# Kernel optimization log

Measured on AMD Instinct MI355X. Metric: run time of the kernel, lower is better.

Reference implementation:

```python
import jax, jax.numpy as jnp
import numpy as np

N_NODES = 50000
N_EDGES = 800000
N_GRAPHS = 50
IN_FEATS = 128
H1_FEATS = 64
OUT_FEATS = 32
GAT_SLOPE = 0.2   # DGL GATConv default negative_slope
LRELU_SLOPE = 0.01  # F.leaky_relu default


def setup_inputs() -> dict:
    key = jax.random.key(0)
    ks = jax.random.split(key, 12)
    x = jax.random.normal(ks[0], (N_NODES, IN_FEATS), jnp.float32)
    src = jax.random.randint(ks[1], (N_EDGES,), 0, N_NODES)
    dst = jax.random.randint(ks[2], (N_EDGES,), 0, N_NODES)
    graph_id = jnp.sort(jax.random.randint(ks[3], (N_NODES,), 0, N_GRAPHS))
    s1 = 1.0 / np.sqrt(IN_FEATS)
    s2 = 1.0 / np.sqrt(H1_FEATS)
    W1 = jax.random.normal(ks[4], (IN_FEATS, H1_FEATS), jnp.float32) * s1
    al1 = jax.random.normal(ks[5], (H1_FEATS,), jnp.float32) * s2
    ar1 = jax.random.normal(ks[6], (H1_FEATS,), jnp.float32) * s2
    b1 = jnp.zeros((H1_FEATS,), jnp.float32)
    W2 = jax.random.normal(ks[7], (H1_FEATS, OUT_FEATS), jnp.float32) * s2
    al2 = jax.random.normal(ks[8], (OUT_FEATS,), jnp.float32) * (1.0 / np.sqrt(OUT_FEATS))
    ar2 = jax.random.normal(ks[9], (OUT_FEATS,), jnp.float32) * (1.0 / np.sqrt(OUT_FEATS))
    b2 = jnp.zeros((OUT_FEATS,), jnp.float32)
    return {"x": x, "src": src, "dst": dst, "graph_id": graph_id,
            "W1": W1, "al1": al1, "ar1": ar1, "b1": b1,
            "W2": W2, "al2": al2, "ar2": ar2, "b2": b2}


def _gat_layer(h, src, dst, W, al, ar, b, n_nodes):
    # single-head DGL GATConv (feat_drop=attn_drop=0, bias added post-aggregation)
    z = h @ W                                   # (N, out)
    el = z @ al                                 # (N,) left attention logits
    er = z @ ar                                 # (N,) right attention logits
    e = jax.nn.leaky_relu(el[src] + er[dst], GAT_SLOPE)     # (E,)
    m = jax.ops.segment_max(e, dst, num_segments=n_nodes)  # per-dst max for stable softmax
    p = jnp.exp(e - m[dst])
    s = jax.ops.segment_sum(p, dst, num_segments=n_nodes)
    alpha = p / s[dst]                          # edge softmax over incoming edges
    out = jax.ops.segment_sum(alpha[:, None] * z[src], dst, num_segments=n_nodes)
    return out + b


def reference(x, src, dst, graph_id, W1, al1, ar1, b1, W2, al2, ar2, b2):
    n = x.shape[0]
    h = jax.nn.leaky_relu(_gat_layer(x, src, dst, W1, al1, ar1, b1, n), LRELU_SLOPE)
    h = jax.nn.leaky_relu(_gat_layer(h, src, dst, W2, al2, ar2, b2, n), LRELU_SLOPE)
    # dgl.mean_nodes: per-graph mean over nodes
    cnt = jax.ops.segment_sum(jnp.ones((n,), h.dtype), graph_id, num_segments=N_GRAPHS)
    pooled = jax.ops.segment_sum(h, graph_id, num_segments=N_GRAPHS) / jnp.maximum(cnt, 1.0)[:, None]
    return pooled
```

## Files before the change

kernel.cpp:

```cpp
#include <hip/hip_runtime.h>
#include <math.h>

#define NN 50000
#define NE 800000
#define NG 50
#define F0 128
#define F1 64
#define F2 32
#define NPB 256
#define NBK 196
#define CHUNK 4096
#define NC 196

__device__ __forceinline__ float lrelu(float v, float slope) {
    return v > 0.0f ? v : v * slope;
}

__global__ __launch_bounds__(256) void gemm1_kernel(
    const float* __restrict__ x, const float* __restrict__ W,
    const float* __restrict__ al, const float* __restrict__ ar,
    float* __restrict__ z, float* __restrict__ el, float* __restrict__ er)
{
    __shared__ float Ws[F0 * F1];
    __shared__ float xs[32][F0];
    int tid = threadIdx.x;
    int r0 = blockIdx.x * 32;

    {
        const float4* W4 = reinterpret_cast<const float4*>(W);
        float4* Ws4 = reinterpret_cast<float4*>(Ws);
        #pragma unroll
        for (int i = 0; i < 8; ++i) Ws4[tid + i * 256] = W4[tid + i * 256];
    }
    {
        float4 zero = {0.f, 0.f, 0.f, 0.f};
        #pragma unroll
        for (int i = 0; i < 4; ++i) {
            int s = tid + i * 256;
            int row = s >> 5, c4 = s & 31;
            int grow = r0 + row;
            float4 v = (grow < NN)
                ? reinterpret_cast<const float4*>(x)[(size_t)grow * 32 + c4] : zero;
            *reinterpret_cast<float4*>(&xs[row][c4 * 4]) = v;
        }
    }
    __syncthreads();

    int j = tid & 63, rg = tid >> 6;
    float acc[8] = {0.f, 0.f, 0.f, 0.f, 0.f, 0.f, 0.f, 0.f};
    for (int k4 = 0; k4 < F0 / 4; ++k4) {
        float w0 = Ws[(k4 * 4 + 0) * F1 + j];
        float w1 = Ws[(k4 * 4 + 1) * F1 + j];
        float w2 = Ws[(k4 * 4 + 2) * F1 + j];
        float w3 = Ws[(k4 * 4 + 3) * F1 + j];
        #pragma unroll
        for (int r = 0; r < 8; ++r) {
            float4 xv = *reinterpret_cast<const float4*>(&xs[rg * 8 + r][k4 * 4]);
            acc[r] = fmaf(xv.x, w0, fmaf(xv.y, w1, fmaf(xv.z, w2, fmaf(xv.w, w3, acc[r]))));
        }
    }

    float a_l = al[j], a_r = ar[j];
    #pragma unroll
    for (int r = 0; r < 8; ++r) {
        int row = r0 + rg * 8 + r;
        if (row < NN) z[(size_t)row * F1 + j] = acc[r];
        float pl = acc[r] * a_l, pr = acc[r] * a_r;
        #pragma unroll
        for (int mm = 1; mm < 64; mm <<= 1) {
            pl += __shfl_xor(pl, mm);
            pr += __shfl_xor(pr, mm);
        }
        if (j == 0 && row < NN) { el[row] = pl; er[row] = pr; }
    }
}

__global__ __launch_bounds__(256) void gemm2_kernel(
    const float* __restrict__ h, const float* __restrict__ W,
    const float* __restrict__ al, const float* __restrict__ ar,
    float* __restrict__ z, float* __restrict__ el, float* __restrict__ er)
{
    __shared__ float Ws[F1 * F2];
    __shared__ float xs[64][F1];
    int tid = threadIdx.x;
    int r0 = blockIdx.x * 64;

    {
        const float4* W4 = reinterpret_cast<const float4*>(W);
        float4* Ws4 = reinterpret_cast<float4*>(Ws);
        #pragma unroll
        for (int i = 0; i < 2; ++i) Ws4[tid + i * 256] = W4[tid + i * 256];
    }
    {
        float4 zero = {0.f, 0.f, 0.f, 0.f};
        #pragma unroll
        for (int i = 0; i < 4; ++i) {
            int s = tid + i * 256;
            int row = s >> 4, c4 = s & 15;
            int grow = r0 + row;
            float4 v = (grow < NN)
                ? reinterpret_cast<const float4*>(h)[(size_t)grow * 16 + c4] : zero;
            *reinterpret_cast<float4*>(&xs[row][c4 * 4]) = v;
        }
    }
    __syncthreads();

    int j = tid & 31, rg = tid >> 5;
    float acc[8] = {0.f, 0.f, 0.f, 0.f, 0.f, 0.f, 0.f, 0.f};
    for (int k4 = 0; k4 < F1 / 4; ++k4) {
        float w0 = Ws[(k4 * 4 + 0) * F2 + j];
        float w1 = Ws[(k4 * 4 + 1) * F2 + j];
        float w2 = Ws[(k4 * 4 + 2) * F2 + j];
        float w3 = Ws[(k4 * 4 + 3) * F2 + j];
        #pragma unroll
        for (int r = 0; r < 8; ++r) {
            float4 xv = *reinterpret_cast<const float4*>(&xs[rg * 8 + r][k4 * 4]);
            acc[r] = fmaf(xv.x, w0, fmaf(xv.y, w1, fmaf(xv.z, w2, fmaf(xv.w, w3, acc[r]))));
        }
    }

    float a_l = al[j], a_r = ar[j];
    #pragma unroll
    for (int r = 0; r < 8; ++r) {
        int row = r0 + rg * 8 + r;
        if (row < NN) z[(size_t)row * F2 + j] = acc[r];
        float pl = acc[r] * a_l, pr = acc[r] * a_r;
        #pragma unroll
        for (int mm = 1; mm < 32; mm <<= 1) {
            pl += __shfl_xor(pl, mm);
            pr += __shfl_xor(pr, mm);
        }
        if (j == 0 && row < NN) { el[row] = pl; er[row] = pr; }
    }
}


__global__ __launch_bounds__(256) void p1_hist_kernel(
    const int* __restrict__ dst, int* __restrict__ hist)
{
    __shared__ int h[NBK];
    int c = blockIdx.x;
    if (threadIdx.x < NBK) h[threadIdx.x] = 0;
    __syncthreads();
    int e0 = c * CHUNK;
    int e1 = (e0 + CHUNK < NE) ? e0 + CHUNK : NE;
    for (int e = e0 + threadIdx.x; e < e1; e += 256)
        atomicAdd(&h[dst[e] >> 8], 1);
    __syncthreads();
    if (threadIdx.x < NBK) hist[threadIdx.x * NC + c] = h[threadIdx.x];
}

__global__ __launch_bounds__(256) void p2a_scan_kernel(
    int* __restrict__ hist, int* __restrict__ btot)
{
    __shared__ int t[256];
    int b = blockIdx.x;
    int v = (threadIdx.x < NC) ? hist[b * NC + threadIdx.x] : 0;
    t[threadIdx.x] = v;
    __syncthreads();
    for (int off = 1; off < 256; off <<= 1) {
        int u = (threadIdx.x >= off) ? t[threadIdx.x - off] : 0;
        __syncthreads();
        t[threadIdx.x] += u;
        __syncthreads();
    }
    if (threadIdx.x < NC) hist[b * NC + threadIdx.x] = t[threadIdx.x] - v;
    if (threadIdx.x == 255) btot[b] = t[255];
}

__global__ __launch_bounds__(256) void p2b_scan_kernel(
    const int* __restrict__ btot, int* __restrict__ bstart, int* __restrict__ row_start)
{
    __shared__ int t[256];
    int v = (threadIdx.x < NBK) ? btot[threadIdx.x] : 0;
    t[threadIdx.x] = v;
    __syncthreads();
    for (int off = 1; off < 256; off <<= 1) {
        int u = (threadIdx.x >= off) ? t[threadIdx.x - off] : 0;
        __syncthreads();
        t[threadIdx.x] += u;
        __syncthreads();
    }
    if (threadIdx.x < NBK) bstart[threadIdx.x] = t[threadIdx.x] - v;
    if (threadIdx.x == NBK) bstart[NBK] = NE;
    if (threadIdx.x == 0) row_start[NN] = NE;
}

__global__ __launch_bounds__(256) void p3_part_kernel(
    const int* __restrict__ src, const int* __restrict__ dst,
    const int* __restrict__ hist, const int* __restrict__ bstart,
    int2* __restrict__ part)
{
    __shared__ int base[NBK];
    __shared__ int cnt[NBK];
    int c = blockIdx.x;
    if (threadIdx.x < NBK) {
        base[threadIdx.x] = hist[threadIdx.x * NC + c] + bstart[threadIdx.x];
        cnt[threadIdx.x] = 0;
    }
    __syncthreads();
    int e0 = c * CHUNK;
    int e1 = (e0 + CHUNK < NE) ? e0 + CHUNK : NE;
    for (int e = e0 + threadIdx.x; e < e1; e += 256) {
        int s = src[e], d = dst[e];
        int b = d >> 8;
        int r = atomicAdd(&cnt[b], 1);
        part[base[b] + r] = make_int2(s, d);
    }
}

__global__ __launch_bounds__(256) void p4_fill_kernel(
    const int2* __restrict__ part, const int* __restrict__ bstart,
    int* __restrict__ row_start, int* __restrict__ srcs)
{
    __shared__ int deg[NPB];
    __shared__ int off[NPB];
    __shared__ int cnt[NPB];
    int b = blockIdx.x;
    int lo = bstart[b], hi = bstart[b + 1];
    deg[threadIdx.x] = 0;
    cnt[threadIdx.x] = 0;
    __syncthreads();
    for (int i = lo + threadIdx.x; i < hi; i += 256)
        atomicAdd(&deg[part[i].y & (NPB - 1)], 1);
    __syncthreads();
    int v = deg[threadIdx.x];
    off[threadIdx.x] = v;
    __syncthreads();
    for (int o = 1; o < 256; o <<= 1) {
        int u = (threadIdx.x >= o) ? off[threadIdx.x - o] : 0;
        __syncthreads();
        off[threadIdx.x] += u;
        __syncthreads();
    }
    int ex = off[threadIdx.x] - v;
    __syncthreads();
    off[threadIdx.x] = ex;
    __syncthreads();
    int node = b * NPB + threadIdx.x;
    if (node < NN) row_start[node] = lo + ex;
    for (int i = lo + threadIdx.x; i < hi; i += 256) {
        int2 e = part[i];
        int n = e.y & (NPB - 1);
        int r = atomicAdd(&cnt[n], 1);
        srcs[lo + off[n] + r] = e.x;
    }
}

__global__ __launch_bounds__(256) void gat_agg64_kernel(
    const int* __restrict__ row_start, const int* __restrict__ srcs,
    const float* __restrict__ el, const float* __restrict__ er,
    const float* __restrict__ z, const float* __restrict__ b,
    float* __restrict__ out, float slope_out)
{
    int node = (blockIdx.x * 256 + threadIdx.x) >> 6;
    if (node >= NN) return;
    int lane = threadIdx.x & 63;
    int g = lane >> 4, c = lane & 15;
    int beg = row_start[node], end = row_start[node + 1];
    float erd = er[node];

    int i0 = beg + lane;
    float v0 = -INFINITY;
    if (i0 < end) v0 = lrelu(el[srcs[i0]] + erd, 0.2f);
    float lm = v0;
    for (int i = i0 + 64; i < end; i += 64)
        lm = fmaxf(lm, lrelu(el[srcs[i]] + erd, 0.2f));
    #pragma unroll
    for (int mm = 1; mm < 64; mm <<= 1) lm = fmaxf(lm, __shfl_xor(lm, mm));

    float preg = 0.f, ls = 0.f;
    if (i0 < end) { preg = __expf(v0 - lm); ls = preg; }
    for (int i = i0 + 64; i < end; i += 64)
        ls += __expf(lrelu(el[srcs[i]] + erd, 0.2f) - lm);
    #pragma unroll
    for (int mm = 1; mm < 64; mm <<= 1) ls += __shfl_xor(ls, mm);
    float inv_s = (ls > 0.f) ? 1.0f / ls : 0.f;

    const float4* z4 = reinterpret_cast<const float4*>(z);
    float4 acc = {0.f, 0.f, 0.f, 0.f};
    for (int ib = beg; ib < end; ib += 4) {
        int i = ib + g;
        int j = i - beg;
        float pv = __shfl(preg, j & 63);
        if (i < end) {
            int sn = srcs[i];
            if (j >= 64) pv = __expf(lrelu(el[sn] + erd, 0.2f) - lm);
            float alpha = pv * inv_s;
            float4 zv = z4[(size_t)sn * 16 + c];
            acc.x = fmaf(alpha, zv.x, acc.x);
            acc.y = fmaf(alpha, zv.y, acc.y);
            acc.z = fmaf(alpha, zv.z, acc.z);
            acc.w = fmaf(alpha, zv.w, acc.w);
        }
    }
    #pragma unroll
    for (int mm = 16; mm < 64; mm <<= 1) {
        acc.x += __shfl_xor(acc.x, mm);
        acc.y += __shfl_xor(acc.y, mm);
        acc.z += __shfl_xor(acc.z, mm);
        acc.w += __shfl_xor(acc.w, mm);
    }
    if (g == 0) {
        float4 bb = reinterpret_cast<const float4*>(b)[c];
        float4 o;
        o.x = lrelu(acc.x + bb.x, slope_out);
        o.y = lrelu(acc.y + bb.y, slope_out);
        o.z = lrelu(acc.z + bb.z, slope_out);
        o.w = lrelu(acc.w + bb.w, slope_out);
        reinterpret_cast<float4*>(out)[(size_t)node * 16 + c] = o;
    }
}

__global__ __launch_bounds__(256) void gat_agg32_kernel(
    const int* __restrict__ row_start, const int* __restrict__ srcs,
    const float* __restrict__ el, const float* __restrict__ er,
    const float* __restrict__ z, const float* __restrict__ b,
    float* __restrict__ out, float slope_out)
{
    int node = (blockIdx.x * 256 + threadIdx.x) >> 5;
    if (node >= NN) return;
    int sub = threadIdx.x & 31;
    int base = threadIdx.x & 32;
    int g = sub >> 3, c = sub & 7;
    int beg = row_start[node], end = row_start[node + 1];
    float erd = er[node];

    int i0 = beg + sub;
    float v0 = -INFINITY;
    if (i0 < end) v0 = lrelu(el[srcs[i0]] + erd, 0.2f);
    float lm = v0;
    for (int i = i0 + 32; i < end; i += 32)
        lm = fmaxf(lm, lrelu(el[srcs[i]] + erd, 0.2f));
    #pragma unroll
    for (int mm = 1; mm < 32; mm <<= 1) lm = fmaxf(lm, __shfl_xor(lm, mm));

    float preg = 0.f, ls = 0.f;
    if (i0 < end) { preg = __expf(v0 - lm); ls = preg; }
    for (int i = i0 + 32; i < end; i += 32)
        ls += __expf(lrelu(el[srcs[i]] + erd, 0.2f) - lm);
    #pragma unroll
    for (int mm = 1; mm < 32; mm <<= 1) ls += __shfl_xor(ls, mm);
    float inv_s = (ls > 0.f) ? 1.0f / ls : 0.f;

    const float4* z4 = reinterpret_cast<const float4*>(z);
    float4 acc = {0.f, 0.f, 0.f, 0.f};
    for (int ib = beg; ib < end; ib += 4) {
        int i = ib + g;
        int j = i - beg;
        float pv = __shfl(preg, base | (j & 31));
        if (i < end) {
            int sn = srcs[i];
            if (j >= 32) pv = __expf(lrelu(el[sn] + erd, 0.2f) - lm);
            float alpha = pv * inv_s;
            float4 zv = z4[(size_t)sn * 8 + c];
            acc.x = fmaf(alpha, zv.x, acc.x);
            acc.y = fmaf(alpha, zv.y, acc.y);
            acc.z = fmaf(alpha, zv.z, acc.z);
            acc.w = fmaf(alpha, zv.w, acc.w);
        }
    }
    #pragma unroll
    for (int mm = 8; mm < 32; mm <<= 1) {
        acc.x += __shfl_xor(acc.x, mm);
        acc.y += __shfl_xor(acc.y, mm);
        acc.z += __shfl_xor(acc.z, mm);
        acc.w += __shfl_xor(acc.w, mm);
    }
    if (g == 0) {
        float4 bb = reinterpret_cast<const float4*>(b)[c];
        float4 o;
        o.x = lrelu(acc.x + bb.x, slope_out);
        o.y = lrelu(acc.y + bb.y, slope_out);
        o.z = lrelu(acc.z + bb.z, slope_out);
        o.w = lrelu(acc.w + bb.w, slope_out);
        reinterpret_cast<float4*>(out)[(size_t)node * 8 + c] = o;
    }
}

__global__ __launch_bounds__(256) void pool_kernel(
    const float* __restrict__ h2, const int* __restrict__ gid, float* __restrict__ out)
{
    int g = blockIdx.x;
    int lo = 0, hi = NN;
    while (lo < hi) { int mid = (lo + hi) >> 1; if (gid[mid] < g) lo = mid + 1; else hi = mid; }
    int start = lo;
    hi = NN;
    while (lo < hi) { int mid = (lo + hi) >> 1; if (gid[mid] < g + 1) lo = mid + 1; else hi = mid; }
    int end = lo;

    int f = threadIdx.x & 31, r = threadIdx.x >> 5;
    float acc = 0.f;
    for (int n = start + r; n < end; n += 8) acc += h2[(size_t)n * F2 + f];
    __shared__ float red[256];
    red[threadIdx.x] = acc;
    __syncthreads();
    for (int st = 128; st >= 32; st >>= 1) {
        if (threadIdx.x < st) red[threadIdx.x] += red[threadIdx.x + st];
        __syncthreads();
    }
    if (threadIdx.x < 32) {
        float cnt = (float)(end - start);
        out[g * F2 + threadIdx.x] = red[threadIdx.x] / fmaxf(cnt, 1.0f);
    }
}

extern "C" void kernel_launch(void* const* d_in, const int* in_sizes, int n_in,
                              void* d_out, int out_size, void* d_ws, size_t ws_size,
                              hipStream_t stream)
{
    const float* x   = (const float*)d_in[0];
    const int*   src = (const int*)d_in[1];
    const int*   dst = (const int*)d_in[2];
    const int*   gid = (const int*)d_in[3];
    const float* W1  = (const float*)d_in[4];
    const float* al1 = (const float*)d_in[5];
    const float* ar1 = (const float*)d_in[6];
    const float* b1  = (const float*)d_in[7];
    const float* W2  = (const float*)d_in[8];
    const float* al2 = (const float*)d_in[9];
    const float* ar2 = (const float*)d_in[10];
    const float* b2  = (const float*)d_in[11];
    float* out = (float*)d_out;

    float* ws   = (float*)d_ws;
    float* z1   = ws;
    float* h1   = z1 + (size_t)NN * F1;
    float* z2   = h1 + (size_t)NN * F1;
    float* h2   = z2 + (size_t)NN * F2;
    float* el   = h2 + (size_t)NN * F2;
    float* er   = el + NN;
    int* row_start = (int*)(er + NN);
    int* srcs      = row_start + NN + 1;
    int* hist      = srcs + NE;
    int* btot      = hist + NBK * NC;
    int* bstart    = btot + NBK;
    int2* part = reinterpret_cast<int2*>(z1);

    p1_hist_kernel<<<NC, 256, 0, stream>>>(dst, hist);
    p2a_scan_kernel<<<NBK, 256, 0, stream>>>(hist, btot);
    p2b_scan_kernel<<<1, 256, 0, stream>>>(btot, bstart, row_start);
    p3_part_kernel<<<NC, 256, 0, stream>>>(src, dst, hist, bstart, part);
    p4_fill_kernel<<<NBK, 256, 0, stream>>>(part, bstart, row_start, srcs);

    gemm1_kernel<<<(NN + 31) / 32, 256, 0, stream>>>(x, W1, al1, ar1, z1, el, er);
    gat_agg64_kernel<<<(NN * 64 + 255) / 256, 256, 0, stream>>>(
        row_start, srcs, el, er, z1, b1, h1, 0.01f);

    gemm2_kernel<<<(NN + 63) / 64, 256, 0, stream>>>(h1, W2, al2, ar2, z2, el, er);
    gat_agg32_kernel<<<(NN * 32 + 255) / 256, 256, 0, stream>>>(
        row_start, srcs, el, er, z2, b2, h2, 0.01f);

    pool_kernel<<<NG, 256, 0, stream>>>(h2, gid, out);
}
```

Before: 286.8 us.

## Fuse histogram into gemm1, drop bucket-scan kernel, unroll aggregation loops

The edge-destination histogram is merged into the first GEMM launch as extra blocks, so both run in one grid. The single-block bucket scan kernel is removed, and each partition/fill block recomputes the 196-entry prefix sum itself. The partition buffer moves out of z1 so it no longer aliases the GEMM output, which is what allows the fusion. The aggregation kernels pre-scale the softmax weights by the inverse sum and process two edges per iteration to expose more memory-level parallelism, at the cost of redundant scan work per block and more register pressure.

```diff
diff --git a/kernel.cpp b/kernel.cpp
--- a/kernel.cpp
+++ b/kernel.cpp
@@ -11,12 +11,15 @@
 #define NBK 196
 #define CHUNK 4096
 #define NC 196
+#define NTILE1 1563
+#define NTILE2 782
 
 __device__ __forceinline__ float lrelu(float v, float slope) {
     return v > 0.0f ? v : v * slope;
 }
 
-__global__ __launch_bounds__(256) void gemm1_kernel(
+__global__ __launch_bounds__(256) void k1_hist_gemm1_kernel(
+    const int* __restrict__ dst, int* __restrict__ hist,
     const float* __restrict__ x, const float* __restrict__ W,
     const float* __restrict__ al, const float* __restrict__ ar,
     float* __restrict__ z, float* __restrict__ el, float* __restrict__ er)
@@ -24,8 +27,22 @@
     __shared__ float Ws[F0 * F1];
     __shared__ float xs[32][F0];
     int tid = threadIdx.x;
-    int r0 = blockIdx.x * 32;
-
+
+    if (blockIdx.x < NC) {
+        int* h = (int*)Ws;
+        int c = blockIdx.x;
+        if (tid < NBK) h[tid] = 0;
+        __syncthreads();
+        int e0 = c * CHUNK;
+        int e1 = (e0 + CHUNK < NE) ? e0 + CHUNK : NE;
+        for (int e = e0 + tid; e < e1; e += 256)
+            atomicAdd(&h[dst[e] >> 8], 1);
+        __syncthreads();
+        if (tid < NBK) hist[tid * NC + c] = h[tid];
+        return;
+    }
+
+    int r0 = (blockIdx.x - NC) * 32;
     {
         const float4* W4 = reinterpret_cast<const float4*>(W);
         float4* Ws4 = reinterpret_cast<float4*>(Ws);
@@ -45,7 +62,6 @@
         }
     }
     __syncthreads();
-
     int j = tid & 63, rg = tid >> 6;
     float acc[8] = {0.f, 0.f, 0.f, 0.f, 0.f, 0.f, 0.f, 0.f};
     for (int k4 = 0; k4 < F0 / 4; ++k4) {
@@ -59,7 +75,6 @@
             acc[r] = fmaf(xv.x, w0, fmaf(xv.y, w1, fmaf(xv.z, w2, fmaf(xv.w, w3, acc[r]))));
         }
     }
-
     float a_l = al[j], a_r = ar[j];
     #pragma unroll
     for (int r = 0; r < 8; ++r) {
@@ -75,81 +90,6 @@
     }
 }
 
-__global__ __launch_bounds__(256) void gemm2_kernel(
-    const float* __restrict__ h, const float* __restrict__ W,
-    const float* __restrict__ al, const float* __restrict__ ar,
-    float* __restrict__ z, float* __restrict__ el, float* __restrict__ er)
-{
-    __shared__ float Ws[F1 * F2];
-    __shared__ float xs[64][F1];
-    int tid = threadIdx.x;
-    int r0 = blockIdx.x * 64;
-
-    {
-        const float4* W4 = reinterpret_cast<const float4*>(W);
-        float4* Ws4 = reinterpret_cast<float4*>(Ws);
-        #pragma unroll
-        for (int i = 0; i < 2; ++i) Ws4[tid + i * 256] = W4[tid + i * 256];
-    }
-    {
-        float4 zero = {0.f, 0.f, 0.f, 0.f};
-        #pragma unroll
-        for (int i = 0; i < 4; ++i) {
-            int s = tid + i * 256;
-            int row = s >> 4, c4 = s & 15;
-            int grow = r0 + row;
-            float4 v = (grow < NN)
-                ? reinterpret_cast<const float4*>(h)[(size_t)grow * 16 + c4] : zero;
-            *reinterpret_cast<float4*>(&xs[row][c4 * 4]) = v;
-        }
-    }
-    __syncthreads();
-
-    int j = tid & 31, rg = tid >> 5;
-    float acc[8] = {0.f, 0.f, 0.f, 0.f, 0.f, 0.f, 0.f, 0.f};
-    for (int k4 = 0; k4 < F1 / 4; ++k4) {
-        float w0 = Ws[(k4 * 4 + 0) * F2 + j];
-        float w1 = Ws[(k4 * 4 + 1) * F2 + j];
-        float w2 = Ws[(k4 * 4 + 2) * F2 + j];
-        float w3 = Ws[(k4 * 4 + 3) * F2 + j];
-        #pragma unroll
-        for (int r = 0; r < 8; ++r) {
-            float4 xv = *reinterpret_cast<const float4*>(&xs[rg * 8 + r][k4 * 4]);
-            acc[r] = fmaf(xv.x, w0, fmaf(xv.y, w1, fmaf(xv.z, w2, fmaf(xv.w, w3, acc[r]))));
-        }
-    }
-
-    float a_l = al[j], a_r = ar[j];
-    #pragma unroll
-    for (int r = 0; r < 8; ++r) {
-        int row = r0 + rg * 8 + r;
-        if (row < NN) z[(size_t)row * F2 + j] = acc[r];
-        float pl = acc[r] * a_l, pr = acc[r] * a_r;
-        #pragma unroll
-        for (int mm = 1; mm < 32; mm <<= 1) {
-            pl += __shfl_xor(pl, mm);
-            pr += __shfl_xor(pr, mm);
-        }
-        if (j == 0 && row < NN) { el[row] = pl; er[row] = pr; }
-    }
-}
-
-
-__global__ __launch_bounds__(256) void p1_hist_kernel(
-    const int* __restrict__ dst, int* __restrict__ hist)
-{
-    __shared__ int h[NBK];
-    int c = blockIdx.x;
-    if (threadIdx.x < NBK) h[threadIdx.x] = 0;
-    __syncthreads();
-    int e0 = c * CHUNK;
-    int e1 = (e0 + CHUNK < NE) ? e0 + CHUNK : NE;
-    for (int e = e0 + threadIdx.x; e < e1; e += 256)
-        atomicAdd(&h[dst[e] >> 8], 1);
-    __syncthreads();
-    if (threadIdx.x < NBK) hist[threadIdx.x * NC + c] = h[threadIdx.x];
-}
-
 __global__ __launch_bounds__(256) void p2a_scan_kernel(
     int* __restrict__ hist, int* __restrict__ btot)
 {
@@ -168,40 +108,33 @@
     if (threadIdx.x == 255) btot[b] = t[255];
 }
 
-__global__ __launch_bounds__(256) void p2b_scan_kernel(
-    const int* __restrict__ btot, int* __restrict__ bstart, int* __restrict__ row_start)
-{
-    __shared__ int t[256];
-    int v = (threadIdx.x < NBK) ? btot[threadIdx.x] : 0;
-    t[threadIdx.x] = v;
-    __syncthreads();
-    for (int off = 1; off < 256; off <<= 1) {
-        int u = (threadIdx.x >= off) ? t[threadIdx.x - off] : 0;
-        __syncthreads();
-        t[threadIdx.x] += u;
-        __syncthreads();
-    }
-    if (threadIdx.x < NBK) bstart[threadIdx.x] = t[threadIdx.x] - v;
-    if (threadIdx.x == NBK) bstart[NBK] = NE;
-    if (threadIdx.x == 0) row_start[NN] = NE;
-}
-
 __global__ __launch_bounds__(256) void p3_part_kernel(
     const int* __restrict__ src, const int* __restrict__ dst,
-    const int* __restrict__ hist, const int* __restrict__ bstart,
+    const int* __restrict__ hist, const int* __restrict__ btot,
     int2* __restrict__ part)
 {
+    __shared__ int t[256];
     __shared__ int base[NBK];
     __shared__ int cnt[NBK];
+    int tid = threadIdx.x;
     int c = blockIdx.x;
-    if (threadIdx.x < NBK) {
-        base[threadIdx.x] = hist[threadIdx.x * NC + c] + bstart[threadIdx.x];
-        cnt[threadIdx.x] = 0;
+    int v = (tid < NBK) ? btot[tid] : 0;
+    t[tid] = v;
+    __syncthreads();
+    for (int off = 1; off < 256; off <<= 1) {
+        int u = (tid >= off) ? t[tid - off] : 0;
+        __syncthreads();
+        t[tid] += u;
+        __syncthreads();
+    }
+    if (tid < NBK) {
+        base[tid] = hist[tid * NC + c] + (t[tid] - v);
+        cnt[tid] = 0;
     }
     __syncthreads();
     int e0 = c * CHUNK;
     int e1 = (e0 + CHUNK < NE) ? e0 + CHUNK : NE;
-    for (int e = e0 + threadIdx.x; e < e1; e += 256) {
+    for (int e = e0 + tid; e < e1; e += 256) {
         int s = src[e], d = dst[e];
         int b = d >> 8;
         int r = atomicAdd(&cnt[b], 1);
@@ -210,36 +143,49 @@
 }
 
 __global__ __launch_bounds__(256) void p4_fill_kernel(
-    const int2* __restrict__ part, const int* __restrict__ bstart,
+    const int2* __restrict__ part, const int* __restrict__ btot,
     int* __restrict__ row_start, int* __restrict__ srcs)
 {
+    __shared__ int t[256];
     __shared__ int deg[NPB];
     __shared__ int off[NPB];
     __shared__ int cnt[NPB];
+    int tid = threadIdx.x;
     int b = blockIdx.x;
-    int lo = bstart[b], hi = bstart[b + 1];
-    deg[threadIdx.x] = 0;
-    cnt[threadIdx.x] = 0;
-    __syncthreads();
-    for (int i = lo + threadIdx.x; i < hi; i += 256)
+    int v = (tid < NBK) ? btot[tid] : 0;
+    t[tid] = v;
+    __syncthreads();
+    for (int o = 1; o < 256; o <<= 1) {
+        int u = (tid >= o) ? t[tid - o] : 0;
+        __syncthreads();
+        t[tid] += u;
+        __syncthreads();
+    }
+    int hi = t[b];
+    int lo = hi - btot[b];
+    if (b == 0 && tid == 0) row_start[NN] = NE;
+    deg[tid] = 0;
+    cnt[tid] = 0;
+    __syncthreads();
+    for (int i = lo + tid; i < hi; i += 256)
         atomicAdd(&deg[part[i].y & (NPB - 1)], 1);
     __syncthreads();
-    int v = deg[threadIdx.x];
-    off[threadIdx.x] = v;
+    int dv = deg[tid];
+    off[tid] = dv;
     __syncthreads();
     for (int o = 1; o < 256; o <<= 1) {
-        int u = (threadIdx.x >= o) ? off[threadIdx.x - o] : 0;
-        __syncthreads();
-        off[threadIdx.x] += u;
-        __syncthreads();
-    }
-    int ex = off[threadIdx.x] - v;
-    __syncthreads();
-    off[threadIdx.x] = ex;
-    __syncthreads();
-    int node = b * NPB + threadIdx.x;
+        int u = (tid >= o) ? off[tid - o] : 0;
+        __syncthreads();
+        off[tid] += u;
+        __syncthreads();
+    }
+    int ex = off[tid] - dv;
+    __syncthreads();
+    off[tid] = ex;
+    __syncthreads();
+    int node = b * NPB + tid;
     if (node < NN) row_start[node] = lo + ex;
-    for (int i = lo + threadIdx.x; i < hi; i += 256) {
+    for (int i = lo + tid; i < hi; i += 256) {
         int2 e = part[i];
         int n = e.y & (NPB - 1);
         int r = atomicAdd(&cnt[n], 1);
@@ -276,22 +222,37 @@
     #pragma unroll
     for (int mm = 1; mm < 64; mm <<= 1) ls += __shfl_xor(ls, mm);
     float inv_s = (ls > 0.f) ? 1.0f / ls : 0.f;
+    preg *= inv_s;
 
     const float4* z4 = reinterpret_cast<const float4*>(z);
     float4 acc = {0.f, 0.f, 0.f, 0.f};
-    for (int ib = beg; ib < end; ib += 4) {
-        int i = ib + g;
-        int j = i - beg;
-        float pv = __shfl(preg, j & 63);
+    int ib = beg;
+    for (; ib + 8 <= end; ib += 8) {
+        int ia = ib + g, ic = ib + 4 + g;
+        int ja = ia - beg, jc = ic - beg;
+        float aa = __shfl(preg, ja & 63);
+        float ac = __shfl(preg, jc & 63);
+        int sna = srcs[ia], snc = srcs[ic];
+        if (ja >= 64) aa = __expf(lrelu(el[sna] + erd, 0.2f) - lm) * inv_s;
+        if (jc >= 64) ac = __expf(lrelu(el[snc] + erd, 0.2f) - lm) * inv_s;
+        float4 zva = z4[(size_t)sna * 16 + c];
+        float4 zvc = z4[(size_t)snc * 16 + c];
+        acc.x = fmaf(aa, zva.x, fmaf(ac, zvc.x, acc.x));
+        acc.y = fmaf(aa, zva.y, fmaf(ac, zvc.y, acc.y));
+        acc.z = fmaf(aa, zva.z, fmaf(ac, zvc.z, acc.z));
+        acc.w = fmaf(aa, zva.w, fmaf(ac, zvc.w, acc.w));
+    }
+    for (; ib < end; ib += 4) {
+        int i = ib + g, jj = i - beg;
+        float aa = __shfl(preg, jj & 63);
         if (i < end) {
             int sn = srcs[i];
-            if (j >= 64) pv = __expf(lrelu(el[sn] + erd, 0.2f) - lm);
-            float alpha = pv * inv_s;
+            if (jj >= 64) aa = __expf(lrelu(el[sn] + erd, 0.2f) - lm) * inv_s;
             float4 zv = z4[(size_t)sn * 16 + c];
-            acc.x = fmaf(alpha, zv.x, acc.x);
-            acc.y = fmaf(alpha, zv.y, acc.y);
-            acc.z = fmaf(alpha, zv.z, acc.z);
-            acc.w = fmaf(alpha, zv.w, acc.w);
+            acc.x = fmaf(aa, zv.x, acc.x);
+            acc.y = fmaf(aa, zv.y, acc.y);
+            acc.z = fmaf(aa, zv.z, acc.z);
+            acc.w = fmaf(aa, zv.w, acc.w);
         }
     }
     #pragma unroll
@@ -342,22 +303,37 @@
     #pragma unroll
     for (int mm = 1; mm < 32; mm <<= 1) ls += __shfl_xor(ls, mm);
     float inv_s = (ls > 0.f) ? 1.0f / ls : 0.f;
+    preg *= inv_s;
 
     const float4* z4 = reinterpret_cast<const float4*>(z);
     float4 acc = {0.f, 0.f, 0.f, 0.f};
-    for (int ib = beg; ib < end; ib += 4) {
-        int i = ib + g;
-        int j = i - beg;
-        float pv = __shfl(preg, base | (j & 31));
+    int ib = beg;
+    for (; ib + 8 <= end; ib += 8) {
+        int ia = ib + g, ic = ib + 4 + g;
+        int ja = ia - beg, jc = ic - beg;
+        float aa = __shfl(preg, base | (ja & 31));
+        float ac = __shfl(preg, base | (jc & 31));
+        int sna = srcs[ia], snc = srcs[ic];
+        if (ja >= 32) aa = __expf(lrelu(el[sna] + erd, 0.2f) - lm) * inv_s;
+        if (jc >= 32) ac = __expf(lrelu(el[snc] + erd, 0.2f) - lm) * inv_s;
+        float4 zva = z4[(size_t)sna * 8 + c];
+        float4 zvc = z4[(size_t)snc * 8 + c];
+        acc.x = fmaf(aa, zva.x, fmaf(ac, zvc.x, acc.x));
+        acc.y = fmaf(aa, zva.y, fmaf(ac, zvc.y, acc.y));
+        acc.z = fmaf(aa, zva.z, fmaf(ac, zvc.z, acc.z));
+        acc.w = fmaf(aa, zva.w, fmaf(ac, zvc.w, acc.w));
+    }
+    for (; ib < end; ib += 4) {
+        int i = ib + g, jj = i - beg;
+        float aa = __shfl(preg, base | (jj & 31));
         if (i < end) {
             int sn = srcs[i];
-            if (j >= 32) pv = __expf(lrelu(el[sn] + erd, 0.2f) - lm);
-            float alpha = pv * inv_s;
+            if (jj >= 32) aa = __expf(lrelu(el[sn] + erd, 0.2f) - lm) * inv_s;
             float4 zv = z4[(size_t)sn * 8 + c];
-            acc.x = fmaf(alpha, zv.x, acc.x);
-            acc.y = fmaf(alpha, zv.y, acc.y);
-            acc.z = fmaf(alpha, zv.z, acc.z);
-            acc.w = fmaf(alpha, zv.w, acc.w);
+            acc.x = fmaf(aa, zv.x, acc.x);
+            acc.y = fmaf(aa, zv.y, acc.y);
+            acc.z = fmaf(aa, zv.z, acc.z);
+            acc.w = fmaf(aa, zv.w, acc.w);
         }
     }
     #pragma unroll
@@ -378,6 +354,62 @@
     }
 }
 
+__global__ __launch_bounds__(256) void gemm2_kernel(
+    const float* __restrict__ h, const float* __restrict__ W,
+    const float* __restrict__ al, const float* __restrict__ ar,
+    float* __restrict__ z, float* __restrict__ el, float* __restrict__ er)
+{
+    __shared__ float Ws[F1 * F2];
+    __shared__ float xs[64][F1];
+    int tid = threadIdx.x;
+    int r0 = blockIdx.x * 64;
+    {
+        const float4* W4 = reinterpret_cast<const float4*>(W);
+        float4* Ws4 = reinterpret_cast<float4*>(Ws);
+        #pragma unroll
+        for (int i = 0; i < 2; ++i) Ws4[tid + i * 256] = W4[tid + i * 256];
+    }
+    {
+        float4 zero = {0.f, 0.f, 0.f, 0.f};
+        #pragma unroll
+        for (int i = 0; i < 4; ++i) {
+            int s = tid + i * 256;
+            int row = s >> 4, c4 = s & 15;
+            int grow = r0 + row;
+            float4 v = (grow < NN)
+                ? reinterpret_cast<const float4*>(h)[(size_t)grow * 16 + c4] : zero;
+            *reinterpret_cast<float4*>(&xs[row][c4 * 4]) = v;
+        }
+    }
+    __syncthreads();
+    int j = tid & 31, rg = tid >> 5;
+    float acc[8] = {0.f, 0.f, 0.f, 0.f, 0.f, 0.f, 0.f, 0.f};
+    for (int k4 = 0; k4 < F1 / 4; ++k4) {
+        float w0 = Ws[(k4 * 4 + 0) * F2 + j];
+        float w1 = Ws[(k4 * 4 + 1) * F2 + j];
+        float w2 = Ws[(k4 * 4 + 2) * F2 + j];
+        float w3 = Ws[(k4 * 4 + 3) * F2 + j];
+        #pragma unroll
+        for (int r = 0; r < 8; ++r) {
+            float4 xv = *reinterpret_cast<const float4*>(&xs[rg * 8 + r][k4 * 4]);
+            acc[r] = fmaf(xv.x, w0, fmaf(xv.y, w1, fmaf(xv.z, w2, fmaf(xv.w, w3, acc[r]))));
+        }
+    }
+    float a_l = al[j], a_r = ar[j];
+    #pragma unroll
+    for (int r = 0; r < 8; ++r) {
+        int row = r0 + rg * 8 + r;
+        if (row < NN) z[(size_t)row * F2 + j] = acc[r];
+        float pl = acc[r] * a_l, pr = acc[r] * a_r;
+        #pragma unroll
+        for (int mm = 1; mm < 32; mm <<= 1) {
+            pl += __shfl_xor(pl, mm);
+            pr += __shfl_xor(pr, mm);
+        }
+        if (j == 0 && row < NN) { el[row] = pl; er[row] = pr; }
+    }
+}
+
 __global__ __launch_bounds__(256) void pool_kernel(
     const float* __restrict__ h2, const int* __restrict__ gid, float* __restrict__ out)
 {
@@ -388,7 +420,6 @@
     hi = NN;
     while (lo < hi) { int mid = (lo + hi) >> 1; if (gid[mid] < g + 1) lo = mid + 1; else hi = mid; }
     int end = lo;
-
     int f = threadIdx.x & 31, r = threadIdx.x >> 5;
     float acc = 0.f;
     for (int n = start + r; n < end; n += 8) acc += h2[(size_t)n * F2 + f];
@@ -434,22 +465,17 @@
     int* srcs      = row_start + NN + 1;
     int* hist      = srcs + NE;
     int* btot      = hist + NBK * NC;
-    int* bstart    = btot + NBK;
-    int2* part = reinterpret_cast<int2*>(z1);
-
-    p1_hist_kernel<<<NC, 256, 0, stream>>>(dst, hist);
+    int2* part     = (int2*)(btot + NBK + 2);
+
+    k1_hist_gemm1_kernel<<<NC + NTILE1, 256, 0, stream>>>(
+        dst, hist, x, W1, al1, ar1, z1, el, er);
     p2a_scan_kernel<<<NBK, 256, 0, stream>>>(hist, btot);
-    p2b_scan_kernel<<<1, 256, 0, stream>>>(btot, bstart, row_start);
-    p3_part_kernel<<<NC, 256, 0, stream>>>(src, dst, hist, bstart, part);
-    p4_fill_kernel<<<NBK, 256, 0, stream>>>(part, bstart, row_start, srcs);
-
-    gemm1_kernel<<<(NN + 31) / 32, 256, 0, stream>>>(x, W1, al1, ar1, z1, el, er);
+    p3_part_kernel<<<NC, 256, 0, stream>>>(src, dst, hist, btot, part);
+    p4_fill_kernel<<<NBK, 256, 0, stream>>>(part, btot, row_start, srcs);
     gat_agg64_kernel<<<(NN * 64 + 255) / 256, 256, 0, stream>>>(
         row_start, srcs, el, er, z1, b1, h1, 0.01f);
-
-    gemm2_kernel<<<(NN + 63) / 64, 256, 0, stream>>>(h1, W2, al2, ar2, z2, el, er);
+    gemm2_kernel<<<NTILE2, 256, 0, stream>>>(h1, W2, al2, ar2, z2, el, er);
     gat_agg32_kernel<<<(NN * 32 + 255) / 256, 256, 0, stream>>>(
         row_start, srcs, el, er, z2, b2, h2, 0.01f);
-
     pool_kernel<<<NG, 256, 0, stream>>>(h2, gid, out);
 }
```

New measurement: 273.7 us. 1.05x faster.
